# Performance work log

Measured on AMD Instinct MI355X. Metric: run time of the kernel, lower is better.

The kernel has to match this reference:

```python
import jax, jax.numpy as jnp
import numpy as np

B, S, H, D, P = 16, 512, 12, 768, 256
TOP_RATE = 0.1
K = int(round(TOP_RATE * S))  # 51, matches round(self.top_rate * hidden_state.size(1))
LN_EPS = 1e-5


def setup_inputs() -> dict:
    key = jax.random.key(0)
    ks = jax.random.split(key, 6)
    return {
        "hidden_state": jax.random.normal(ks[0], (B, S, D), dtype=jnp.float32),
        "attention": jax.random.normal(ks[1], (B, H, S, S), dtype=jnp.float32),
        "length": S,  # uniform valid length (scalar int)
        # node_trans: Linear(D, P)
        "W_node": jax.random.normal(ks[2], (D, P), dtype=jnp.float32) * 0.02,
        "b_node": jnp.zeros((P,), dtype=jnp.float32),
        # node_eta parameter, initialized to 0 (self.node_eta.data.fill_(0))
        "node_eta": jnp.zeros((1,), dtype=jnp.float32),
        # fc: Linear(P, P)
        "W_fc": jax.random.normal(ks[3], (P, P), dtype=jnp.float32) * 0.02,
        "b_fc": jnp.zeros((P,), dtype=jnp.float32),
        # LayerNorm(P)
        "ln_gamma": jnp.ones((P,), dtype=jnp.float32),
        "ln_beta": jnp.zeros((P,), dtype=jnp.float32),
    }


def reference(hidden_state, attention, W_node, b_node, node_eta, W_fc, b_fc,
              ln_gamma, ln_beta, length):
    # average attention over heads: [B, S, S]
    avg_atten = attention.mean(axis=1)
    # per-target-node top-k neighbors
    vals, idx = jax.lax.top_k(avg_atten, K)  # [B, S, K]
    # edge mask replicating softmax(where(v>0, v, -1e9)) followed by nonzero():
    # entries at -1e9 underflow to exactly 0 in fp32 softmax iff the row has a
    # positive value; otherwise the softmax is uniform and all edges survive.
    keep = vals > 0.0
    row_has_pos = keep.any(axis=-1, keepdims=True)
    keep = jnp.where(row_has_pos, keep, True)            # [B, S, K] (>=1 True per row)
    keepf = keep.astype(hidden_state.dtype)[..., None]   # [B, S, K, 1]

    # node_trans on all nodes: [B, S, P]
    h = hidden_state @ W_node + b_node

    # gather source-node features h[b, idx[b, t, j], :] -> [B, S, K, P]
    gathered = jax.vmap(lambda hb, ib: hb[ib])(h, idx)

    # reduce='mean': edge weight w=1, mailbox mean over kept incoming edges
    h_agg = (gathered * keepf).sum(axis=2) / keepf.sum(axis=2)

    eta = node_eta[0]
    new_h = eta * h + (1.0 - eta) * h_agg                # [B, S, P]

    # dgl.mean_nodes: mean over the `length` nodes of each sub-graph (=S here)
    out = new_h.mean(axis=1)                             # [B, P]

    # fc(dropout(tanh(out))) with dropout in eval mode (identity)
    out = jnp.tanh(out) @ W_fc + b_fc

    # LayerNorm
    mu = out.mean(axis=-1, keepdims=True)
    var = ((out - mu) ** 2).mean(axis=-1, keepdims=True)
    out = (out - mu) / jnp.sqrt(var + LN_EPS) * ln_gamma + ln_beta
    return out
```

## Files before the change

### kernel.cpp

```cpp
#include <hip/hip_runtime.h>
#include <math.h>

#define B_ 16
#define S_ 512
#define H_ 12
#define D_ 768
#define P_ 256
#define K_ 51
#define CH_ 16
#define NCHUNK_ (S_/CH_)

#define WAVE_SYNC() asm volatile("s_waitcnt lgkmcnt(0)" ::: "memory")

__device__ __forceinline__ unsigned okey(float f) {
  unsigned u = __float_as_uint(f);
  return (u & 0x80000000u) ? ~u : (u | 0x80000000u);
}

__global__ __launch_bounds__(256) void k1_topk_weights(
    const float* __restrict__ attn, float* __restrict__ w) {
  const int tid = threadIdx.x;
  const int wv = tid >> 6;
  const int lane = tid & 63;
  const int bt = blockIdx.x * 4 + wv;
  const int b = bt >> 9;
  const int t = bt & (S_ - 1);

  __shared__ __align__(16) unsigned hist[4][256];

  *(uint4*)&hist[wv][4 * lane] = uint4{0u, 0u, 0u, 0u};

  const float* base = attn + (((size_t)b * H_) * S_ + t) * S_;
  float a[8] = {0.f, 0.f, 0.f, 0.f, 0.f, 0.f, 0.f, 0.f};
  #pragma unroll
  for (int h = 0; h < H_; ++h) {
    const float* r = base + (size_t)h * (S_ * S_);
    const float4 u = *(const float4*)(r + 4 * lane);
    const float4 v = *(const float4*)(r + 256 + 4 * lane);
    a[0] += u.x; a[1] += u.y; a[2] += u.z; a[3] += u.w;
    a[4] += v.x; a[5] += v.y; a[6] += v.z; a[7] += v.w;
  }
  unsigned k[8];
  #pragma unroll
  for (int i = 0; i < 8; ++i) {
    a[i] *= (1.0f / (float)H_);
    k[i] = okey(a[i]);
  }

  int p = 0;
  #pragma unroll
  for (int i = 0; i < 8; ++i) p += __popcll(__ballot(a[i] > 0.f));

  bool sel[8];
  float invcnt;
  if (p >= 1 && p < K_) {
    #pragma unroll
    for (int i = 0; i < 8; ++i) sel[i] = (a[i] > 0.f);
    invcnt = 1.0f / (float)p;
  } else {
    unsigned prefix = 0;
    int remaining = K_;
    int tieCnt = 0;
    bool exited = false;
    unsigned exitm = 0;
    for (int pass = 0; pass < 4; ++pass) {
      const int shift = 24 - 8 * pass;
      const unsigned pm = (pass == 0) ? 0u : (0xFFFFFFFFu << (shift + 8));
      WAVE_SYNC();
      #pragma unroll
      for (int i = 0; i < 8; ++i)
        if ((k[i] & pm) == prefix)
          atomicAdd(&hist[wv][(k[i] >> shift) & 255u], 1u);
      WAVE_SYNC();
      const uint4 c4 = *(uint4*)&hist[wv][4 * lane];
      *(uint4*)&hist[wv][4 * lane] = uint4{0u, 0u, 0u, 0u};
      const unsigned loc = c4.x + c4.y + c4.z + c4.w;
      unsigned suf = loc;
      #pragma unroll
      for (int off = 1; off < 64; off <<= 1) {
        const unsigned vv = __shfl_down(suf, off, 64);
        if (lane + off < 64) suf += vv;
      }
      const unsigned after = suf - loc;
      const unsigned s3 = after + c4.w;
      const unsigned s2 = s3 + c4.z;
      const unsigned s1 = s2 + c4.y;
      const unsigned s0 = s1 + c4.x;
      const unsigned rem = (unsigned)remaining;
      int dig = 0, abv = 0, tie = 0;
      bool found = false;
      if (s0 >= rem && s1 < rem)         { dig = 4*lane+0; abv = (int)s1;    tie = (int)(s0 - s1);    found = true; }
      else if (s1 >= rem && s2 < rem)    { dig = 4*lane+1; abv = (int)s2;    tie = (int)(s1 - s2);    found = true; }
      else if (s2 >= rem && s3 < rem)    { dig = 4*lane+2; abv = (int)s3;    tie = (int)(s2 - s3);    found = true; }
      else if (s3 >= rem && after < rem) { dig = 4*lane+3; abv = (int)after; tie = (int)(s3 - after); found = true; }
      const unsigned long long fm = __ballot(found);
      const int src = __ffsll((unsigned long long)fm) - 1;
      dig = __shfl(dig, src, 64);
      abv = __shfl(abv, src, 64);
      tie = __shfl(tie, src, 64);
      prefix |= ((unsigned)dig) << shift;
      remaining -= abv;
      tieCnt = tie;
      if (tieCnt == remaining) {
        exited = true;
        exitm = (shift == 0) ? 0xFFFFFFFFu : (0xFFFFFFFFu << shift);
        break;
      }
    }
    if (exited) {
      #pragma unroll
      for (int i = 0; i < 8; ++i) sel[i] = (k[i] & exitm) >= prefix;
    } else {
      const unsigned T = prefix;
      unsigned long long m[8];
      #pragma unroll
      for (int i = 0; i < 8; ++i) m[i] = __ballot(k[i] == T);
      const unsigned long long lt = ((unsigned long long)1 << lane) - 1ull;
      int fh = 0;
      #pragma unroll
      for (int i = 0; i < 4; ++i) fh += __popcll(m[i]);
      #pragma unroll
      for (int i = 0; i < 8; ++i) {
        sel[i] = (k[i] > T);
        if (k[i] == T) {
          int r = 0;
          if (i < 4) {
            #pragma unroll
            for (int i2 = 0; i2 < 4; ++i2) r += __popcll(m[i2] & lt);
            for (int i2 = 0; i2 < i; ++i2) r += (int)((m[i2] >> lane) & 1ull);
          } else {
            r = fh;
            #pragma unroll
            for (int i2 = 4; i2 < 8; ++i2) r += __popcll(m[i2] & lt);
            for (int i2 = 4; i2 < i; ++i2) r += (int)((m[i2] >> lane) & 1ull);
          }
          if (r < remaining) sel[i] = true;
        }
      }
    }
    invcnt = 1.0f / (float)K_;
  }

  float* wrow = w + b * S_;
  #pragma unroll
  for (int i = 0; i < 8; ++i) {
    const int col = (i < 4) ? (4 * lane + i) : (256 + 4 * lane + (i - 4));
    if (sel[i]) atomicAdd(&wrow[col], invcnt);
  }
}

__global__ __launch_bounds__(192) void k2_weighted_sum(
    const float* __restrict__ hidden, const float* __restrict__ w,
    const float* __restrict__ node_eta, float* __restrict__ x) {
  const int chunk = blockIdx.x;
  const int b = blockIdx.y;
  const int tid = threadIdx.x;
  __shared__ float coef[CH_];
  if (tid < CH_) {
    const float eta = node_eta[0];
    const float wv = w[b * S_ + chunk * CH_ + tid];
    coef[tid] = (eta + (1.0f - eta) * wv) * (1.0f / (float)S_);
  }
  __syncthreads();
  const float* hb = hidden + ((size_t)b * S_ + (size_t)chunk * CH_) * D_ + 4 * tid;
  float4 acc = make_float4(0.f, 0.f, 0.f, 0.f);
  #pragma unroll
  for (int s = 0; s < CH_; ++s) {
    const float4 v = *(const float4*)(hb + (size_t)s * D_);
    const float c = coef[s];
    acc.x += c * v.x; acc.y += c * v.y; acc.z += c * v.z; acc.w += c * v.w;
  }
  float* xp = x + b * D_ + 4 * tid;
  atomicAdd(xp + 0, acc.x);
  atomicAdd(xp + 1, acc.y);
  atomicAdd(xp + 2, acc.z);
  atomicAdd(xp + 3, acc.w);
}

__global__ __launch_bounds__(256) void k3a_tanh_matvec(
    const float* __restrict__ x, const float* __restrict__ W_node,
    const float* __restrict__ b_node, float* __restrict__ tbuf) {
  const int j = blockIdx.x;
  const int b = blockIdx.y;
  const int tid = threadIdx.x;
  const int pp = tid & 15;
  const int g = tid >> 4;
  __shared__ float xs[D_];
  __shared__ float part[16][32];
  for (int d = tid; d < D_; d += 256) xs[d] = x[b * D_ + d];
  __syncthreads();
  const float* Wp = W_node + 32 * j + 2 * pp;
  float2 acc = make_float2(0.f, 0.f);
  const int d0 = 48 * g;
  #pragma unroll 8
  for (int dd = 0; dd < 48; ++dd) {
    const int d = d0 + dd;
    const float2 wv = *(const float2*)(Wp + (size_t)d * P_);
    const float xv = xs[d];
    acc.x += xv * wv.x; acc.y += xv * wv.y;
  }
  *(float2*)&part[g][2 * pp] = acc;
  __syncthreads();
  if (tid < 32) {
    float s = 0.f;
    #pragma unroll
    for (int gg = 0; gg < 16; ++gg) s += part[gg][tid];
    const int pcol = 32 * j + tid;
    tbuf[b * P_ + pcol] = tanhf(s + b_node[pcol]);
  }
}

__global__ __launch_bounds__(256) void k3b_fc(
    const float* __restrict__ tbuf, const float* __restrict__ W_fc,
    const float* __restrict__ b_fc, float* __restrict__ obuf) {
  const int j = blockIdx.x;
  const int b = blockIdx.y;
  const int tid = threadIdx.x;
  const int pp = tid & 31;
  const int g = tid >> 5;
  __shared__ float ts[P_];
  __shared__ float part[8][64];
  ts[tid] = tbuf[b * P_ + tid];
  __syncthreads();
  const float* Wp = W_fc + 64 * j + 2 * pp;
  float2 acc = make_float2(0.f, 0.f);
  const int q0 = 32 * g;
  #pragma unroll 8
  for (int qq = 0; qq < 32; ++qq) {
    const int q = q0 + qq;
    const float2 wv = *(const float2*)(Wp + (size_t)q * P_);
    const float tv = ts[q];
    acc.x += tv * wv.x; acc.y += tv * wv.y;
  }
  *(float2*)&part[g][2 * pp] = acc;
  __syncthreads();
  if (tid < 64) {
    float s = 0.f;
    #pragma unroll
    for (int gg = 0; gg < 8; ++gg) s += part[gg][tid];
    const int pcol = 64 * j + tid;
    obuf[b * P_ + pcol] = s + b_fc[pcol];
  }
}

__global__ __launch_bounds__(256) void k3c_layernorm(
    const float* __restrict__ obuf, const float* __restrict__ gamma,
    const float* __restrict__ beta, float* __restrict__ out) {
  const int b = blockIdx.x;
  const int tid = threadIdx.x;
  __shared__ float red[4];
  const float o = obuf[b * P_ + tid];
  float s = o;
  #pragma unroll
  for (int off = 32; off > 0; off >>= 1) s += __shfl_down(s, off, 64);
  const int wave = tid >> 6, lane = tid & 63;
  if (lane == 0) red[wave] = s;
  __syncthreads();
  const float mu = (red[0] + red[1] + red[2] + red[3]) * (1.0f / (float)P_);
  __syncthreads();
  const float dv = o - mu;
  float s2 = dv * dv;
  #pragma unroll
  for (int off = 32; off > 0; off >>= 1) s2 += __shfl_down(s2, off, 64);
  if (lane == 0) red[wave] = s2;
  __syncthreads();
  const float var = (red[0] + red[1] + red[2] + red[3]) * (1.0f / (float)P_);
  const float inv = 1.0f / sqrtf(var + 1e-5f);
  out[b * P_ + tid] = dv * inv * gamma[tid] + beta[tid];
}

extern "C" void kernel_launch(void* const* d_in, const int* in_sizes, int n_in,
                              void* d_out, int out_size, void* d_ws, size_t ws_size,
                              hipStream_t stream) {
  (void)in_sizes; (void)n_in; (void)out_size; (void)ws_size;
  const float* hidden   = (const float*)d_in[0];
  const float* attn     = (const float*)d_in[1];
  const float* W_node   = (const float*)d_in[3];
  const float* b_node   = (const float*)d_in[4];
  const float* node_eta = (const float*)d_in[5];
  const float* W_fc     = (const float*)d_in[6];
  const float* b_fc     = (const float*)d_in[7];
  const float* gamma    = (const float*)d_in[8];
  const float* beta     = (const float*)d_in[9];
  float* out = (float*)d_out;

  float* w    = (float*)d_ws;
  float* x    = w + B_ * S_;
  float* tbuf = x + B_ * D_;
  float* obuf = tbuf + B_ * P_;
  hipMemsetAsync(d_ws, 0, (size_t)(B_ * S_ + B_ * D_) * sizeof(float), stream);

  k1_topk_weights<<<(B_ * S_) / 4, 256, 0, stream>>>(attn, w);
  k2_weighted_sum<<<dim3(NCHUNK_, B_), 192, 0, stream>>>(hidden, w, node_eta, x);
  k3a_tanh_matvec<<<dim3(8, B_), 256, 0, stream>>>(x, W_node, b_node, tbuf);
  k3b_fc<<<dim3(4, B_), 256, 0, stream>>>(tbuf, W_fc, b_fc, obuf);
  k3c_layernorm<<<B_, 256, 0, stream>>>(obuf, gamma, beta, out);
}
```

Baseline: 340.7 us.

## Fuse fc matvec with layernorm and pack top-k selection into bitmask

Merges the fc matvec and LayerNorm kernels into one kernel, with one block per batch row computing all 256 outputs directly. This removes a launch and the intermediate obuf round trip. The top-k kernel now keeps its selection flags in a bitmask instead of a bool array and gets a minimum-blocks launch bound, aimed at lowering register pressure and raising occupancy. The fused fc kernel runs only 16 blocks, each doing a serial 256-step loop, so it exposes less parallelism than the earlier 4x16 grid.

```diff
diff --git a/kernel.cpp b/kernel.cpp
--- a/kernel.cpp
+++ b/kernel.cpp
@@ -17,7 +17,7 @@
   return (u & 0x80000000u) ? ~u : (u | 0x80000000u);
 }
 
-__global__ __launch_bounds__(256) void k1_topk_weights(
+__global__ __launch_bounds__(256, 5) void k1_topk_weights(
     const float* __restrict__ attn, float* __restrict__ w) {
   const int tid = threadIdx.x;
   const int wv = tid >> 6;
@@ -51,11 +51,11 @@
   #pragma unroll
   for (int i = 0; i < 8; ++i) p += __popcll(__ballot(a[i] > 0.f));
 
-  bool sel[8];
+  unsigned selm = 0;
   float invcnt;
   if (p >= 1 && p < K_) {
     #pragma unroll
-    for (int i = 0; i < 8; ++i) sel[i] = (a[i] > 0.f);
+    for (int i = 0; i < 8; ++i) selm |= (a[i] > 0.f) ? (1u << i) : 0u;
     invcnt = 1.0f / (float)p;
   } else {
     unsigned prefix = 0;
@@ -109,7 +109,7 @@
     }
     if (exited) {
       #pragma unroll
-      for (int i = 0; i < 8; ++i) sel[i] = (k[i] & exitm) >= prefix;
+      for (int i = 0; i < 8; ++i) selm |= ((k[i] & exitm) >= prefix) ? (1u << i) : 0u;
     } else {
       const unsigned T = prefix;
       unsigned long long m[8];
@@ -121,7 +121,7 @@
       for (int i = 0; i < 4; ++i) fh += __popcll(m[i]);
       #pragma unroll
       for (int i = 0; i < 8; ++i) {
-        sel[i] = (k[i] > T);
+        bool sel = (k[i] > T);
         if (k[i] == T) {
           int r = 0;
           if (i < 4) {
@@ -134,8 +134,9 @@
             for (int i2 = 4; i2 < 8; ++i2) r += __popcll(m[i2] & lt);
             for (int i2 = 4; i2 < i; ++i2) r += (int)((m[i2] >> lane) & 1ull);
           }
-          if (r < remaining) sel[i] = true;
+          if (r < remaining) sel = true;
         }
+        selm |= sel ? (1u << i) : 0u;
       }
     }
     invcnt = 1.0f / (float)K_;
@@ -145,7 +146,7 @@
   #pragma unroll
   for (int i = 0; i < 8; ++i) {
     const int col = (i < 4) ? (4 * lane + i) : (256 + 4 * lane + (i - 4));
-    if (sel[i]) atomicAdd(&wrow[col], invcnt);
+    if ((selm >> i) & 1u) atomicAdd(&wrow[col], invcnt);
   }
 }
 
@@ -210,46 +211,20 @@
   }
 }
 
-__global__ __launch_bounds__(256) void k3b_fc(
+__global__ __launch_bounds__(256) void k3bc_fc_ln(
     const float* __restrict__ tbuf, const float* __restrict__ W_fc,
-    const float* __restrict__ b_fc, float* __restrict__ obuf) {
-  const int j = blockIdx.x;
-  const int b = blockIdx.y;
-  const int tid = threadIdx.x;
-  const int pp = tid & 31;
-  const int g = tid >> 5;
-  __shared__ float ts[P_];
-  __shared__ float part[8][64];
-  ts[tid] = tbuf[b * P_ + tid];
-  __syncthreads();
-  const float* Wp = W_fc + 64 * j + 2 * pp;
-  float2 acc = make_float2(0.f, 0.f);
-  const int q0 = 32 * g;
-  #pragma unroll 8
-  for (int qq = 0; qq < 32; ++qq) {
-    const int q = q0 + qq;
-    const float2 wv = *(const float2*)(Wp + (size_t)q * P_);
-    const float tv = ts[q];
-    acc.x += tv * wv.x; acc.y += tv * wv.y;
-  }
-  *(float2*)&part[g][2 * pp] = acc;
-  __syncthreads();
-  if (tid < 64) {
-    float s = 0.f;
-    #pragma unroll
-    for (int gg = 0; gg < 8; ++gg) s += part[gg][tid];
-    const int pcol = 64 * j + tid;
-    obuf[b * P_ + pcol] = s + b_fc[pcol];
-  }
-}
-
-__global__ __launch_bounds__(256) void k3c_layernorm(
-    const float* __restrict__ obuf, const float* __restrict__ gamma,
+    const float* __restrict__ b_fc, const float* __restrict__ gamma,
     const float* __restrict__ beta, float* __restrict__ out) {
   const int b = blockIdx.x;
   const int tid = threadIdx.x;
+  __shared__ float ts[P_];
   __shared__ float red[4];
-  const float o = obuf[b * P_ + tid];
+  ts[tid] = tbuf[b * P_ + tid];
+  __syncthreads();
+  float o = b_fc[tid];
+  #pragma unroll 16
+  for (int q = 0; q < P_; ++q) o += ts[q] * W_fc[q * P_ + tid];
+
   float s = o;
   #pragma unroll
   for (int off = 32; off > 0; off >>= 1) s += __shfl_down(s, off, 64);
@@ -287,12 +262,10 @@
   float* w    = (float*)d_ws;
   float* x    = w + B_ * S_;
   float* tbuf = x + B_ * D_;
-  float* obuf = tbuf + B_ * P_;
   hipMemsetAsync(d_ws, 0, (size_t)(B_ * S_ + B_ * D_) * sizeof(float), stream);
 
   k1_topk_weights<<<(B_ * S_) / 4, 256, 0, stream>>>(attn, w);
   k2_weighted_sum<<<dim3(NCHUNK_, B_), 192, 0, stream>>>(hidden, w, node_eta, x);
   k3a_tanh_matvec<<<dim3(8, B_), 256, 0, stream>>>(x, W_node, b_node, tbuf);
-  k3b_fc<<<dim3(4, B_), 256, 0, stream>>>(tbuf, W_fc, b_fc, obuf);
-  k3c_layernorm<<<B_, 256, 0, stream>>>(obuf, gamma, beta, out);
-}
+  k3bc_fc_ln<<<B_, 256, 0, stream>>>(tbuf, W_fc, b_fc, gamma, beta, out);
+}
```

New measurement: 355.6 us. +4.4%, slower.
